# Performance work log

Hardware: AMD Instinct MI355X
Metric: run time of the kernel (lower is better)

The kernel has to match this reference:

```python
import jax, jax.numpy as jnp
import numpy as np

V, D, L, H, T = 32000, 1024, 4, 16, 1024
DH = D // H
SCALE = DH ** -0.5
FF = 4 * D
R = 2  # n_rounds


def setup_inputs() -> dict:
    key = jax.random.key(0)
    ks = iter(jax.random.split(key, 32))
    s = 0.02
    nrm = lambda shape: jax.random.normal(next(ks), shape, dtype=jnp.float32) * s
    inp = {
        "x": jax.random.randint(next(ks), (2, T), 0, V),
        "embed": nrm((V, D)),
        "pos_embed": nrm((T, D)),
        "Wqkv": nrm((L, R, 3 * D, D)),
        "bqkv": jnp.zeros((L, R, 3 * D), jnp.float32),
        "Wo": nrm((L, D, D)),
        "bo": jnp.zeros((L, D), jnp.float32),
        "Wg": nrm((L, D, 2 * D)),
        "bg": jnp.zeros((L, D), jnp.float32),
        "ln1_g": jnp.ones((L, D), jnp.float32),
        "ln1_b": jnp.zeros((L, D), jnp.float32),
        "W1": nrm((L, FF, D)),
        "b1": jnp.zeros((L, FF), jnp.float32),
        "W2": nrm((L, D, FF)),
        "b2": jnp.zeros((L, D), jnp.float32),
        "ln2_g": jnp.ones((L, D), jnp.float32),
        "ln2_b": jnp.zeros((L, D), jnp.float32),
        "lnf_g": jnp.ones((D,), jnp.float32),
        "lnf_b": jnp.zeros((D,), jnp.float32),
    }
    return inp


def _ln(h, g, b, eps=1e-5):
    m = jnp.mean(h, axis=-1, keepdims=True)
    v = jnp.mean((h - m) ** 2, axis=-1, keepdims=True)
    return (h - m) * jax.lax.rsqrt(v + eps) * g + b


def _attend(h, W, b, mask):
    B, Tq, _ = h.shape
    qkv = (h @ W.T + b).reshape(B, Tq, 3, H, DH)
    q, k, v = qkv[:, :, 0], qkv[:, :, 1], qkv[:, :, 2]  # [B,T,H,DH]
    scores = jnp.einsum("bqhd,bkhd->bhqk", q, k) * SCALE
    scores = jnp.where(mask, scores, -jnp.inf)
    a = jax.nn.softmax(scores, axis=-1)
    return jnp.einsum("bhqk,bkhd->bqhd", a, v).reshape(B, Tq, D)


def reference(x, embed, pos_embed, Wqkv, bqkv, Wo, bo, Wg, bg,
              ln1_g, ln1_b, W1, b1, W2, b2, ln2_g, ln2_b, lnf_g, lnf_b):
    B, Tq = x.shape
    mask = jnp.tril(jnp.ones((Tq, Tq), dtype=bool))
    h = embed[x] + pos_embed[jnp.arange(Tq)]
    for l in range(L):
        n1 = _ln(h, ln1_g[l], ln1_b[l])
        pred = _attend(n1, Wqkv[l, 0], bqkv[l, 0], mask)
        cum = pred
        out = pred
        # boosted round 2: attend on residual, gate the correction
        corr = _attend(n1 - cum, Wqkv[l, 1], bqkv[l, 1], mask)
        gate = jax.nn.sigmoid(jnp.concatenate([cum, corr], axis=-1) @ Wg[l].T + bg[l])
        gated = gate * corr
        out = out + gated
        h = h + (out @ Wo[l].T + bo[l])
        n2 = _ln(h, ln2_g[l], ln2_b[l])
        ff = jax.nn.gelu(n2 @ W1[l].T + b1[l], approximate=False) @ W2[l].T + b2[l]
        h = h + ff
    return _ln(h, lnf_g, lnf_b) @ embed.T  # tied head, no bias
```

## Files before the change

kernel.cpp:

```cpp
#include <hip/hip_runtime.h>
#include <math.h>

#define D_  1024
#define T_  1024
#define B_  2
#define H_  16
#define DH_ 64
#define L_  4
#define FF_ 4096
#define V_  32000
#define M_  2048

typedef _Float16 f16;
typedef _Float16 f16x8 __attribute__((ext_vector_type(8)));
typedef _Float16 f16x4 __attribute__((ext_vector_type(4)));
typedef _Float16 f16x2 __attribute__((ext_vector_type(2)));
typedef float    fx4  __attribute__((ext_vector_type(4)));

__global__ __launch_bounds__(256) void f2h_k(const float* __restrict__ in, f16* __restrict__ out) {
    const long i = ((long)blockIdx.x * 256 + threadIdx.x) * 4;
    const float4 v = *(const float4*)(in + i);
    f16x4 o = { (f16)v.x, (f16)v.y, (f16)v.z, (f16)v.w };
    *(f16x4*)(out + i) = o;
}

__global__ __launch_bounds__(256) void embed_k(const int* __restrict__ x, const float* __restrict__ emb,
                                               const float* __restrict__ pos, float* __restrict__ h) {
    const long m = blockIdx.x;
    const int  t = threadIdx.x;
    const long tok = x[m];
    const long pt  = m & (T_ - 1);
    const float4 e = ((const float4*)(emb + tok * D_))[t];
    const float4 p = ((const float4*)(pos + pt * D_))[t];
    ((float4*)(h + m * D_))[t] = make_float4(e.x + p.x, e.y + p.y, e.z + p.z, e.w + p.w);
}

__global__ __launch_bounds__(256) void ln_k(const float* __restrict__ x, const float* __restrict__ g,
                                            const float* __restrict__ b, float* __restrict__ of,
                                            f16* __restrict__ oh) {
    const long m = blockIdx.x;
    const int  t = threadIdx.x;
    const int  wave = t >> 6, lane = t & 63;
    __shared__ float red1[4], red2[4];
    const float4 v = ((const float4*)(x + m * D_))[t];
    float s = v.x + v.y + v.z + v.w;
#pragma unroll
    for (int off = 32; off; off >>= 1) s += __shfl_xor(s, off, 64);
    if (lane == 0) red1[wave] = s;
    __syncthreads();
    const float mean = (red1[0] + red1[1] + red1[2] + red1[3]) * (1.0f / 1024.0f);
    const float d0 = v.x - mean, d1 = v.y - mean, d2 = v.z - mean, d3 = v.w - mean;
    float s2 = d0 * d0 + d1 * d1 + d2 * d2 + d3 * d3;
#pragma unroll
    for (int off = 32; off; off >>= 1) s2 += __shfl_xor(s2, off, 64);
    if (lane == 0) red2[wave] = s2;
    __syncthreads();
    const float var  = (red2[0] + red2[1] + red2[2] + red2[3]) * (1.0f / 1024.0f);
    const float rstd = rsqrtf(var + 1e-5f);
    const float4 gv = ((const float4*)g)[t];
    const float4 bv = ((const float4*)b)[t];
    const float o0 = d0 * rstd * gv.x + bv.x;
    const float o1 = d1 * rstd * gv.y + bv.y;
    const float o2 = d2 * rstd * gv.z + bv.z;
    const float o3 = d3 * rstd * gv.w + bv.w;
    if (of) ((float4*)(of + m * D_))[t] = make_float4(o0, o1, o2, o3);
    if (oh) { f16x4 o = { (f16)o0, (f16)o1, (f16)o2, (f16)o3 }; *(f16x4*)(oh + m * D_ + t * 4) = o; }
}

__global__ __launch_bounds__(256) void sub_k(const float* __restrict__ a, const float* __restrict__ b,
                                             f16* __restrict__ o) {
    const long i = ((long)blockIdx.x * 256 + threadIdx.x) * 4;
    const float4 va = *(const float4*)(a + i);
    const float4 vb = *(const float4*)(b + i);
    f16x4 o4 = { (f16)(va.x - vb.x), (f16)(va.y - vb.y), (f16)(va.z - vb.z), (f16)(va.w - vb.w) };
    *(f16x4*)(o + i) = o4;
}

__global__ __launch_bounds__(256) void cat_k(const float* __restrict__ p, const float* __restrict__ c,
                                             f16* __restrict__ o) {
    const long i = ((long)blockIdx.x * 256 + threadIdx.x) * 4;
    const long m = i >> 11;
    const int  j = (int)(i & 2047);
    const float* src = (j < 1024) ? (p + m * 1024 + j) : (c + m * 1024 + (j - 1024));
    const float4 v = *(const float4*)src;
    f16x4 o4 = { (f16)v.x, (f16)v.y, (f16)v.z, (f16)v.w };
    *(f16x4*)(o + i) = o4;
}

__global__ __launch_bounds__(256) void gate_k(const float* __restrict__ p, const float* __restrict__ c,
                                              const float* __restrict__ gl, f16* __restrict__ o) {
    const long i = ((long)blockIdx.x * 256 + threadIdx.x) * 4;
    const float4 vp = *(const float4*)(p + i);
    const float4 vc = *(const float4*)(c + i);
    const float4 vg = *(const float4*)(gl + i);
    const float s0 = 1.0f / (1.0f + __expf(-vg.x));
    const float s1 = 1.0f / (1.0f + __expf(-vg.y));
    const float s2 = 1.0f / (1.0f + __expf(-vg.z));
    const float s3 = 1.0f / (1.0f + __expf(-vg.w));
    f16x4 o4 = { (f16)(vp.x + s0 * vc.x), (f16)(vp.y + s1 * vc.y),
                 (f16)(vp.z + s2 * vc.z), (f16)(vp.w + s3 * vc.w) };
    *(f16x4*)(o + i) = o4;
}

template<int BN>
__global__ __launch_bounds__(256)
void gemm_bt(const f16* __restrict__ A, const f16* __restrict__ Wt,
             const float* __restrict__ bias, const float* __restrict__ resid,
             float* __restrict__ Cf, f16* __restrict__ Ch,
             int N, int K, int gelu) {
    __shared__ __align__(16) f16 As[3][128 * 32];
    __shared__ __align__(16) f16 Bs[3][BN * 32];
    const int tid  = threadIdx.x;
    const int wave = tid >> 6;
    const int lane = tid & 63;

    const int nbm = gridDim.y;
    const int nbn = gridDim.x;
    int bi = blockIdx.y * nbn + blockIdx.x;
    const int nwg = nbm * nbn;
    if ((nwg & 7) == 0) bi = (bi & 7) * (nwg >> 3) + (bi >> 3);
    const long bm = bi % nbm;
    const long bn = bi / nbm;

    const int wm = (wave >> 1) * 64;
    const int wn = (wave & 1) * (BN / 2);
    constexpr int NJ = BN / 32;

    fx4 acc[4][NJ] = {};

    const int c0 = wave * 2;
    const int r0 = c0 * 16 + (lane >> 2);
    const int cc = ((lane & 3) ^ ((lane >> 3) & 3)) * 8;
    const f16* a0 = A + ((long)bm * 128 + r0) * K + cc;
    const f16* a1 = A + ((long)bm * 128 + r0 + 16) * K + cc;

    const f16* b0;
    const f16* b1 = nullptr;
    if constexpr (BN == 128) {
        b0 = Wt + ((long)bn * 128 + r0) * K + cc;
        b1 = Wt + ((long)bn * 128 + r0 + 16) * K + cc;
    } else {
        b0 = Wt + ((long)bn * 64 + wave * 16 + (lane >> 2)) * K + cc;
    }

    const int NT = K >> 5;

    auto STAGE = [&](int kt) {
        const int k0 = kt * 32;
        const int bf3 = kt % 3;
        __builtin_amdgcn_global_load_lds((const __attribute__((address_space(1))) void*)(a0 + k0),
                                         (__attribute__((address_space(3))) void*)&As[bf3][c0 * 512], 16, 0, 0);
        __builtin_amdgcn_global_load_lds((const __attribute__((address_space(1))) void*)(a1 + k0),
                                         (__attribute__((address_space(3))) void*)&As[bf3][(c0 + 1) * 512], 16, 0, 0);
        if constexpr (BN == 128) {
            __builtin_amdgcn_global_load_lds((const __attribute__((address_space(1))) void*)(b0 + k0),
                                             (__attribute__((address_space(3))) void*)&Bs[bf3][c0 * 512], 16, 0, 0);
            __builtin_amdgcn_global_load_lds((const __attribute__((address_space(1))) void*)(b1 + k0),
                                             (__attribute__((address_space(3))) void*)&Bs[bf3][(c0 + 1) * 512], 16, 0, 0);
        } else {
            __builtin_amdgcn_global_load_lds((const __attribute__((address_space(1))) void*)(b0 + k0),
                                             (__attribute__((address_space(3))) void*)&Bs[bf3][wave * 512], 16, 0, 0);
        }
    };

    STAGE(0);
    if (NT > 1) STAGE(1);

    const int lm = lane & 15;
    const int g  = lane >> 4;
    const int koff = (g ^ ((lm >> 1) & 3)) * 8;
    for (int t = 0; t < NT; ++t) {
        if (t + 2 < NT) STAGE(t + 2);
        const int rem = NT - 1 - t;
        if constexpr (BN == 128) {
            if (rem >= 2)      asm volatile("s_waitcnt vmcnt(8)" ::: "memory");
            else if (rem == 1) asm volatile("s_waitcnt vmcnt(4)" ::: "memory");
            else               asm volatile("s_waitcnt vmcnt(0)" ::: "memory");
        } else {
            if (rem >= 2)      asm volatile("s_waitcnt vmcnt(6)" ::: "memory");
            else if (rem == 1) asm volatile("s_waitcnt vmcnt(3)" ::: "memory");
            else               asm volatile("s_waitcnt vmcnt(0)" ::: "memory");
        }
        __builtin_amdgcn_s_barrier();
        __builtin_amdgcn_sched_barrier(0);

        const f16* as = As[t % 3];
        const f16* bs = Bs[t % 3];
        f16x8 af[4], bf[NJ];
#pragma unroll
        for (int i = 0; i < 4; ++i)
            af[i] = *(const f16x8*)&as[(wm + i * 16 + lm) * 32 + koff];
#pragma unroll
        for (int j = 0; j < NJ; ++j)
            bf[j] = *(const f16x8*)&bs[(wn + j * 16 + lm) * 32 + koff];
#pragma unroll
        for (int i = 0; i < 4; ++i)
#pragma unroll
            for (int j = 0; j < NJ; ++j)
                acc[i][j] = __builtin_amdgcn_mfma_f32_16x16x32_f16(af[i], bf[j], acc[i][j], 0, 0, 0);

        asm volatile("s_waitcnt lgkmcnt(0)" ::: "memory");
        __builtin_amdgcn_sched_barrier(0);
        __builtin_amdgcn_s_barrier();
    }

    const long gr_base = bm * 128 + wm + (lane >> 4) * 4;
    const long gc_base = bn * BN + wn + (lane & 15);
#pragma unroll
    for (int i = 0; i < 4; ++i) {
#pragma unroll
        for (int j = 0; j < NJ; ++j) {
            const long gc = gc_base + j * 16;
            const float bv = bias ? bias[gc] : 0.0f;
#pragma unroll
            for (int r = 0; r < 4; ++r) {
                const long gr = gr_base + i * 16 + r;
                float v = acc[i][j][r] + bv;
                if (gelu) v = 0.5f * v * (1.0f + erff(v * 0.70710678118654752f));
                else if (resid) v += resid[gr * (long)N + gc];
                if (Cf) Cf[gr * (long)N + gc] = v;
                if (Ch) Ch[gr * (long)N + gc] = (f16)v;
            }
        }
    }
}

__global__ __launch_bounds__(256) void fattn_k(const f16* __restrict__ qkv, float* __restrict__ out) {
    __shared__ __align__(16) f16 Ks[64 * 72];
    __shared__ __align__(16) f16 Vt[64 * 72];
    __shared__ __align__(16) f16 Pw[4][16 * 72];
    const int tid  = threadIdx.x;
    const int w    = tid >> 6;
    const int lane = tid & 63;
    const int b  = blockIdx.z, h = blockIdx.y;
    const int qt = (gridDim.x - 1) - blockIdx.x;
    const int q0w = qt * 64 + w * 16;
    const int g  = lane >> 4;
    const int lm = lane & 15;

    const long qrow = ((long)(b * T_ + q0w + lm)) * (3 * D_) + h * DH_;
    f16x8 af_q[2];
    af_q[0] = *(const f16x8*)(qkv + qrow + g * 8);
    af_q[1] = *(const f16x8*)(qkv + qrow + 32 + g * 8);

    float m_r[4], l_r[4];
    fx4 acc_o[4] = {};
#pragma unroll
    for (int r = 0; r < 4; ++r) { m_r[r] = -INFINITY; l_r[r] = 0.0f; }

    const int srow = tid >> 2;
    const int scol = (tid & 3) * 16;
    const long kbase = ((long)(b * T_)) * (3 * D_) + D_ + h * DH_ + scol;
    const int vm  = tid >> 3;
    const int vd0 = (tid & 7) * 8;
    const long vbase = ((long)(b * T_)) * (3 * D_) + 2 * D_ + h * DH_ + vd0;

    f16x8 kr0, kr1, vr0, vr1;
    {
        const f16* ks = qkv + kbase + (long)srow * (3 * D_);
        kr0 = *(const f16x8*)(ks);
        kr1 = *(const f16x8*)(ks + 8);
        const f16* va = qkv + vbase + (long)(2 * vm) * (3 * D_);
        vr0 = *(const f16x8*)(va);
        vr1 = *(const f16x8*)(va + 3 * D_);
    }

    const int nkb = qt + 1;
    for (int it = 0; it < nkb; ++it) {
        const int kb = it * 64;
        __syncthreads();
        *(f16x8*)&Ks[srow * 72 + scol]     = kr0;
        *(f16x8*)&Ks[srow * 72 + scol + 8] = kr1;
#pragma unroll
        for (int j = 0; j < 8; ++j) {
            const int d = vd0 + j;
            const int col = (2 * vm) ^ (((d >> 2) & 7) << 3);
            f16x2 pr = { vr0[j], vr1[j] };
            *(f16x2*)&Vt[d * 72 + col] = pr;
        }
        __syncthreads();

        if (it + 1 < nkb) {
            const int kb2 = kb + 64;
            const f16* ks = qkv + kbase + (long)(kb2 + srow) * (3 * D_);
            kr0 = *(const f16x8*)(ks);
            kr1 = *(const f16x8*)(ks + 8);
            const f16* va = qkv + vbase + (long)(kb2 + 2 * vm) * (3 * D_);
            vr0 = *(const f16x8*)(va);
            vr1 = *(const f16x8*)(va + 3 * D_);
        }

        fx4 sc[4];
#pragma unroll
        for (int kt = 0; kt < 4; ++kt) {
            fx4 c = {};
#pragma unroll
            for (int kk = 0; kk < 2; ++kk) {
                f16x8 bf = *(const f16x8*)&Ks[(kt * 16 + lm) * 72 + kk * 32 + g * 8];
                c = __builtin_amdgcn_mfma_f32_16x16x32_f16(af_q[kk], bf, c, 0, 0, 0);
            }
            sc[kt] = c * 0.125f;
        }
        if (kb == qt * 64) {
#pragma unroll
            for (int kt = 0; kt < 4; ++kt) {
                const int key_g = kb + kt * 16 + lm;
#pragma unroll
                for (int r = 0; r < 4; ++r)
                    if (key_g > q0w + g * 4 + r) sc[kt][r] = -INFINITY;
            }
        }

        float mnew[4], pscale[4];
#pragma unroll
        for (int r = 0; r < 4; ++r) {
            float tm = fmaxf(fmaxf(sc[0][r], sc[1][r]), fmaxf(sc[2][r], sc[3][r]));
#pragma unroll
            for (int off = 8; off; off >>= 1) tm = fmaxf(tm, __shfl_xor(tm, off, 64));
            mnew[r]   = fmaxf(m_r[r], tm);
            pscale[r] = __expf(m_r[r] - mnew[r]);
        }
        float psum[4] = {};
#pragma unroll
        for (int kt = 0; kt < 4; ++kt) {
#pragma unroll
            for (int r = 0; r < 4; ++r) {
                const float p = __expf(sc[kt][r] - mnew[r]);
                sc[kt][r] = p;
                psum[r] += p;
            }
        }
#pragma unroll
        for (int r = 0; r < 4; ++r) {
#pragma unroll
            for (int off = 8; off; off >>= 1) psum[r] += __shfl_xor(psum[r], off, 64);
            l_r[r] = l_r[r] * pscale[r] + psum[r];
            m_r[r] = mnew[r];
        }
#pragma unroll
        for (int nt = 0; nt < 4; ++nt)
#pragma unroll
            for (int r = 0; r < 4; ++r) acc_o[nt][r] *= pscale[r];

        f16* P = Pw[w];
#pragma unroll
        for (int kt = 0; kt < 4; ++kt)
#pragma unroll
            for (int r = 0; r < 4; ++r)
                P[(g * 4 + r) * 72 + kt * 16 + lm] = (f16)sc[kt][r];

#pragma unroll
        for (int kc = 0; kc < 2; ++kc) {
            f16x8 ap = *(const f16x8*)&P[lm * 72 + kc * 32 + g * 8];
#pragma unroll
            for (int nt = 0; nt < 4; ++nt) {
                const int d = nt * 16 + lm;
                const int col = (kc * 32 + g * 8) ^ (((d >> 2) & 7) << 3);
                f16x8 bv = *(const f16x8*)&Vt[d * 72 + col];
                acc_o[nt] = __builtin_amdgcn_mfma_f32_16x16x32_f16(ap, bv, acc_o[nt], 0, 0, 0);
            }
        }
    }

    const long obase = ((long)(b * T_ + q0w + g * 4)) * D_ + h * DH_ + lm;
#pragma unroll
    for (int r = 0; r < 4; ++r) {
        const float inv = 1.0f / l_r[r];
#pragma unroll
        for (int nt = 0; nt < 4; ++nt)
            out[obase + (long)r * D_ + nt * 16] = acc_o[nt][r] * inv;
    }
}

extern "C" void kernel_launch(void* const* d_in, const int* in_sizes, int n_in,
                              void* d_out, int out_size, void* d_ws, size_t ws_size,
                              hipStream_t stream) {
    const int*   x    = (const int*)d_in[0];
    const float* emb  = (const float*)d_in[1];
    const float* pos  = (const float*)d_in[2];
    const float* Wqkv = (const float*)d_in[3];
    const float* bqkv = (const float*)d_in[4];
    const float* Wo   = (const float*)d_in[5];
    const float* bo   = (const float*)d_in[6];
    const float* Wg   = (const float*)d_in[7];
    const float* bg   = (const float*)d_in[8];
    const float* ln1g = (const float*)d_in[9];
    const float* ln1b = (const float*)d_in[10];
    const float* W1   = (const float*)d_in[11];
    const float* b1   = (const float*)d_in[12];
    const float* W2   = (const float*)d_in[13];
    const float* b2   = (const float*)d_in[14];
    const float* ln2g = (const float*)d_in[15];
    const float* ln2b = (const float*)d_in[16];
    const float* lnfg = (const float*)d_in[17];
    const float* lnfb = (const float*)d_in[18];
    float* out = (float*)d_out;

    char* ws = (char*)d_ws;
    size_t off = 0;
    auto alloc = [&](size_t bytes) -> void* {
        off = (off + 255) & ~(size_t)255;
        void* p = ws + off;
        off += bytes;
        return p;
    };
    float* h    = (float*)alloc((size_t)M_ * D_ * 4);
    float* n1f  = (float*)alloc((size_t)M_ * D_ * 4);
    float* pred = (float*)alloc((size_t)M_ * D_ * 4);
    float* corr = (float*)alloc((size_t)M_ * D_ * 4);
    float* glin = (float*)alloc((size_t)M_ * D_ * 4);
    f16* qkvh  = (f16*)alloc((size_t)M_ * 3 * D_ * 2);
    f16* ab    = (f16*)alloc((size_t)M_ * D_ * 2);
    f16* catb  = (f16*)alloc((size_t)M_ * 2 * D_ * 2);
    f16* ffh   = (f16*)alloc((size_t)M_ * FF_ * 2);
    f16* embh  = (f16*)alloc((size_t)V_ * D_ * 2);
    f16* wqkvh = (f16*)alloc((size_t)L_ * 2 * 3 * D_ * D_ * 2);
    f16* woh   = (f16*)alloc((size_t)L_ * D_ * D_ * 2);
    f16* wgh   = (f16*)alloc((size_t)L_ * D_ * 2 * D_ * 2);
    f16* w1h   = (f16*)alloc((size_t)L_ * FF_ * D_ * 2);
    f16* w2h   = (f16*)alloc((size_t)L_ * D_ * FF_ * 2);

    auto cvt = [&](const float* src, f16* dst, long n) {
        f2h_k<<<dim3((unsigned)(n / 1024)), dim3(256), 0, stream>>>(src, dst);
    };
    cvt(emb,  embh,  (long)V_ * D_);
    cvt(Wqkv, wqkvh, (long)L_ * 2 * 3 * D_ * D_);
    cvt(Wo,   woh,   (long)L_ * D_ * D_);
    cvt(Wg,   wgh,   (long)L_ * D_ * 2 * D_);
    cvt(W1,   w1h,   (long)L_ * FF_ * D_);
    cvt(W2,   w2h,   (long)L_ * D_ * FF_);

    embed_k<<<dim3(M_), dim3(256), 0, stream>>>(x, emb, pos, h);

    auto gemm = [&](const f16* A, const f16* Wt, const float* bias, const float* resid,
                    float* Cf, f16* Ch, int N, int K, int gelu) {
        if (N <= 1024)
            gemm_bt<64><<<dim3(N / 64, M_ / 128), dim3(256), 0, stream>>>(A, Wt, bias, resid, Cf, Ch, N, K, gelu);
        else
            gemm_bt<128><<<dim3(N / 128, M_ / 128), dim3(256), 0, stream>>>(A, Wt, bias, resid, Cf, Ch, N, K, gelu);
    };

    for (int l = 0; l < L_; ++l) {
        ln_k<<<dim3(M_), 256, 0, stream>>>(h, ln1g + l * D_, ln1b + l * D_, n1f, ab);
        gemm(ab, wqkvh + (size_t)(l * 2 + 0) * 3 * D_ * D_, bqkv + (l * 2 + 0) * 3 * D_,
             nullptr, nullptr, qkvh, 3 * D_, D_, 0);
        fattn_k<<<dim3(T_ / 64, H_, B_), 256, 0, stream>>>(qkvh, pred);
        sub_k<<<dim3(M_ * D_ / 1024), 256, 0, stream>>>(n1f, pred, ab);
        gemm(ab, wqkvh + (size_t)(l * 2 + 1) * 3 * D_ * D_, bqkv + (l * 2 + 1) * 3 * D_,
             nullptr, nullptr, qkvh, 3 * D_, D_, 0);
        fattn_k<<<dim3(T_ / 64, H_, B_), 256, 0, stream>>>(qkvh, corr);
        cat_k<<<dim3(M_ * 2 * D_ / 1024), 256, 0, stream>>>(pred, corr, catb);
        gemm(catb, wgh + (size_t)l * D_ * 2 * D_, bg + l * D_, nullptr, glin, nullptr, D_, 2 * D_, 0);
        gate_k<<<dim3(M_ * D_ / 1024), 256, 0, stream>>>(pred, corr, glin, ab);
        gemm(ab, woh + (size_t)l * D_ * D_, bo + l * D_, h, h, nullptr, D_, D_, 0);
        ln_k<<<dim3(M_), 256, 0, stream>>>(h, ln2g + l * D_, ln2b + l * D_, nullptr, ab);
        gemm(ab, w1h + (size_t)l * FF_ * D_, b1 + l * FF_, nullptr, nullptr, ffh, FF_, D_, 1);
        gemm(ffh, w2h + (size_t)l * D_ * FF_, b2 + l * D_, h, h, nullptr, D_, FF_, 0);
    }
    ln_k<<<dim3(M_), 256, 0, stream>>>(h, lnfg, lnfb, nullptr, ab);
    gemm(ab, embh, nullptr, nullptr, out, nullptr, V_, D_, 0);
}
```

Baseline: 2.200 ms.

## Vectorize GEMM epilogue via LDS transpose; use 128-key attention tiles with causal skip

The GEMM epilogue now stages each 16x16 accumulator tile through per-wave LDS scratch. Each lane then writes 4 contiguous outputs with vector loads and stores for bias, residual, fp32 and fp16 outputs, replacing scattered scalar stores. The flash attention kernel processes 128 keys per iteration instead of 64, halving barrier and loop overhead. It also skips MFMA and softmax work for fully masked 16-key subtiles on the diagonal block. This costs more LDS and registers per block and extra waitcnt syncs in the epilogue, and could reduce occupancy.

```diff
diff --git a/kernel.cpp b/kernel.cpp
--- a/kernel.cpp
+++ b/kernel.cpp
@@ -204,31 +204,51 @@
         __builtin_amdgcn_s_barrier();
     }
 
-    const long gr_base = bm * 128 + wm + (lane >> 4) * 4;
-    const long gc_base = bn * BN + wn + (lane & 15);
+    float* esc = (float*)&As[0][0] + (size_t)wave * 320;
+    const int erow = lane >> 2;
+    const int ecg  = (lane & 3) * 4;
+    const long gr0 = bm * 128 + wm;
+    const long gc0 = bn * BN + wn;
 #pragma unroll
     for (int i = 0; i < 4; ++i) {
 #pragma unroll
         for (int j = 0; j < NJ; ++j) {
-            const long gc = gc_base + j * 16;
-            const float bv = bias ? bias[gc] : 0.0f;
-#pragma unroll
-            for (int r = 0; r < 4; ++r) {
-                const long gr = gr_base + i * 16 + r;
-                float v = acc[i][j][r] + bv;
-                if (gelu) v = 0.5f * v * (1.0f + erff(v * 0.70710678118654752f));
-                else if (resid) v += resid[gr * (long)N + gc];
-                if (Cf) Cf[gr * (long)N + gc] = v;
-                if (Ch) Ch[gr * (long)N + gc] = (f16)v;
+#pragma unroll
+            for (int r = 0; r < 4; ++r)
+                esc[(g * 4 + r) * 20 + lm] = acc[i][j][r];
+            asm volatile("s_waitcnt lgkmcnt(0)" ::: "memory");
+            __builtin_amdgcn_sched_barrier(0);
+            const fx4 q = *(const fx4*)&esc[erow * 20 + ecg];
+            asm volatile("s_waitcnt lgkmcnt(0)" ::: "memory");
+            __builtin_amdgcn_sched_barrier(0);
+            const long row = gr0 + i * 16 + erow;
+            const long col = gc0 + j * 16 + ecg;
+            fx4 v = q;
+            if (bias) {
+                const fx4 b4 = *(const fx4*)&bias[col];
+                v[0] += b4[0]; v[1] += b4[1]; v[2] += b4[2]; v[3] += b4[3];
+            }
+            if (gelu) {
+#pragma unroll
+                for (int e = 0; e < 4; ++e)
+                    v[e] = 0.5f * v[e] * (1.0f + erff(v[e] * 0.70710678118654752f));
+            } else if (resid) {
+                const fx4 rz = *(const fx4*)&resid[row * (long)N + col];
+                v[0] += rz[0]; v[1] += rz[1]; v[2] += rz[2]; v[3] += rz[3];
+            }
+            if (Cf) *(fx4*)&Cf[row * (long)N + col] = v;
+            if (Ch) {
+                f16x4 hq = { (f16)v[0], (f16)v[1], (f16)v[2], (f16)v[3] };
+                *(f16x4*)&Ch[row * (long)N + col] = hq;
             }
         }
     }
 }
 
 __global__ __launch_bounds__(256) void fattn_k(const f16* __restrict__ qkv, float* __restrict__ out) {
-    __shared__ __align__(16) f16 Ks[64 * 72];
-    __shared__ __align__(16) f16 Vt[64 * 72];
-    __shared__ __align__(16) f16 Pw[4][16 * 72];
+    __shared__ __align__(16) f16 Ks[128 * 72];
+    __shared__ __align__(16) f16 Vt[64 * 136];
+    __shared__ __align__(16) f16 Pw[4][16 * 136];
     const int tid  = threadIdx.x;
     const int w    = tid >> 6;
     const int lane = tid & 63;
@@ -248,73 +268,95 @@
 #pragma unroll
     for (int r = 0; r < 4; ++r) { m_r[r] = -INFINITY; l_r[r] = 0.0f; }
 
-    const int srow = tid >> 2;
-    const int scol = (tid & 3) * 16;
-    const long kbase = ((long)(b * T_)) * (3 * D_) + D_ + h * DH_ + scol;
-    const int vm  = tid >> 3;
-    const int vd0 = (tid & 7) * 8;
+    const int krow = tid >> 1;
+    const int kdh  = (tid & 1) * 32;
+    const long kbase = ((long)(b * T_)) * (3 * D_) + D_ + h * DH_ + kdh;
+    const int vm  = tid >> 2;
+    const int vd0 = (tid & 3) * 16;
     const long vbase = ((long)(b * T_)) * (3 * D_) + 2 * D_ + h * DH_ + vd0;
 
-    f16x8 kr0, kr1, vr0, vr1;
+    const int nit = (qt >> 1) + 1;
+
+    f16x8 kr0, kr1, kr2, kr3, vr0, vr1, vr2, vr3;
     {
-        const f16* ks = qkv + kbase + (long)srow * (3 * D_);
+        const f16* ks = qkv + kbase + (long)krow * (3 * D_);
         kr0 = *(const f16x8*)(ks);
         kr1 = *(const f16x8*)(ks + 8);
+        kr2 = *(const f16x8*)(ks + 16);
+        kr3 = *(const f16x8*)(ks + 24);
         const f16* va = qkv + vbase + (long)(2 * vm) * (3 * D_);
         vr0 = *(const f16x8*)(va);
-        vr1 = *(const f16x8*)(va + 3 * D_);
-    }
-
-    const int nkb = qt + 1;
-    for (int it = 0; it < nkb; ++it) {
-        const int kb = it * 64;
+        vr1 = *(const f16x8*)(va + 8);
+        vr2 = *(const f16x8*)(va + 3 * D_);
+        vr3 = *(const f16x8*)(va + 3 * D_ + 8);
+    }
+
+    for (int it = 0; it < nit; ++it) {
+        const int kb = it * 128;
         __syncthreads();
-        *(f16x8*)&Ks[srow * 72 + scol]     = kr0;
-        *(f16x8*)&Ks[srow * 72 + scol + 8] = kr1;
-#pragma unroll
-        for (int j = 0; j < 8; ++j) {
-            const int d = vd0 + j;
+        *(f16x8*)&Ks[krow * 72 + kdh]      = kr0;
+        *(f16x8*)&Ks[krow * 72 + kdh + 8]  = kr1;
+        *(f16x8*)&Ks[krow * 72 + kdh + 16] = kr2;
+        *(f16x8*)&Ks[krow * 72 + kdh + 24] = kr3;
+#pragma unroll
+        for (int jj = 0; jj < 16; ++jj) {
+            const int d = vd0 + jj;
+            const f16 va_ = (jj < 8) ? vr0[jj] : vr1[jj - 8];
+            const f16 vb_ = (jj < 8) ? vr2[jj] : vr3[jj - 8];
             const int col = (2 * vm) ^ (((d >> 2) & 7) << 3);
-            f16x2 pr = { vr0[j], vr1[j] };
-            *(f16x2*)&Vt[d * 72 + col] = pr;
+            f16x2 pr = { va_, vb_ };
+            *(f16x2*)&Vt[d * 136 + col] = pr;
         }
         __syncthreads();
 
-        if (it + 1 < nkb) {
-            const int kb2 = kb + 64;
-            const f16* ks = qkv + kbase + (long)(kb2 + srow) * (3 * D_);
+        if (it + 1 < nit) {
+            const int kb2 = kb + 128;
+            const f16* ks = qkv + kbase + (long)(kb2 + krow) * (3 * D_);
             kr0 = *(const f16x8*)(ks);
             kr1 = *(const f16x8*)(ks + 8);
+            kr2 = *(const f16x8*)(ks + 16);
+            kr3 = *(const f16x8*)(ks + 24);
             const f16* va = qkv + vbase + (long)(kb2 + 2 * vm) * (3 * D_);
             vr0 = *(const f16x8*)(va);
-            vr1 = *(const f16x8*)(va + 3 * D_);
-        }
-
-        fx4 sc[4];
-#pragma unroll
-        for (int kt = 0; kt < 4; ++kt) {
-            fx4 c = {};
-#pragma unroll
-            for (int kk = 0; kk < 2; ++kk) {
-                f16x8 bf = *(const f16x8*)&Ks[(kt * 16 + lm) * 72 + kk * 32 + g * 8];
-                c = __builtin_amdgcn_mfma_f32_16x16x32_f16(af_q[kk], bf, c, 0, 0, 0);
-            }
-            sc[kt] = c * 0.125f;
-        }
-        if (kb == qt * 64) {
-#pragma unroll
-            for (int kt = 0; kt < 4; ++kt) {
-                const int key_g = kb + kt * 16 + lm;
-#pragma unroll
-                for (int r = 0; r < 4; ++r)
-                    if (key_g > q0w + g * 4 + r) sc[kt][r] = -INFINITY;
+            vr1 = *(const f16x8*)(va + 8);
+            vr2 = *(const f16x8*)(va + 3 * D_);
+            vr3 = *(const f16x8*)(va + 3 * D_ + 8);
+        }
+
+        const int qmax = q0w + 15;
+        int nact = qmax - kb + 1; if (nact > 128) nact = 128;
+        const int nkt = (nact + 15) >> 4;
+        const int nkc = (nact + 31) >> 5;
+        const bool diag = (kb + 127 > q0w);
+
+        fx4 sc[8];
+#pragma unroll
+        for (int kt = 0; kt < 8; ++kt) {
+            if (kt < nkt) {
+                fx4 c = {};
+#pragma unroll
+                for (int kk = 0; kk < 2; ++kk) {
+                    f16x8 bf = *(const f16x8*)&Ks[(kt * 16 + lm) * 72 + kk * 32 + g * 8];
+                    c = __builtin_amdgcn_mfma_f32_16x16x32_f16(af_q[kk], bf, c, 0, 0, 0);
+                }
+                c *= 0.125f;
+                if (diag) {
+                    const int key_g = kb + kt * 16 + lm;
+#pragma unroll
+                    for (int r = 0; r < 4; ++r)
+                        if (key_g > q0w + g * 4 + r) c[r] = -INFINITY;
+                }
+                sc[kt] = c;
             }
         }
 
         float mnew[4], pscale[4];
 #pragma unroll
         for (int r = 0; r < 4; ++r) {
-            float tm = fmaxf(fmaxf(sc[0][r], sc[1][r]), fmaxf(sc[2][r], sc[3][r]));
+            float tm = -INFINITY;
+#pragma unroll
+            for (int kt = 0; kt < 8; ++kt)
+                if (kt < nkt) tm = fmaxf(tm, sc[kt][r]);
 #pragma unroll
             for (int off = 8; off; off >>= 1) tm = fmaxf(tm, __shfl_xor(tm, off, 64));
             mnew[r]   = fmaxf(m_r[r], tm);
@@ -322,12 +364,14 @@
         }
         float psum[4] = {};
 #pragma unroll
-        for (int kt = 0; kt < 4; ++kt) {
-#pragma unroll
-            for (int r = 0; r < 4; ++r) {
-                const float p = __expf(sc[kt][r] - mnew[r]);
-                sc[kt][r] = p;
-                psum[r] += p;
+        for (int kt = 0; kt < 8; ++kt) {
+            if (kt < nkt) {
+#pragma unroll
+                for (int r = 0; r < 4; ++r) {
+                    const float p = __expf(sc[kt][r] - mnew[r]);
+                    sc[kt][r] = p;
+                    psum[r] += p;
+                }
             }
         }
 #pragma unroll
@@ -344,20 +388,29 @@
 
         f16* P = Pw[w];
 #pragma unroll
-        for (int kt = 0; kt < 4; ++kt)
-#pragma unroll
-            for (int r = 0; r < 4; ++r)
-                P[(g * 4 + r) * 72 + kt * 16 + lm] = (f16)sc[kt][r];
-
-#pragma unroll
-        for (int kc = 0; kc < 2; ++kc) {
-            f16x8 ap = *(const f16x8*)&P[lm * 72 + kc * 32 + g * 8];
-#pragma unroll
-            for (int nt = 0; nt < 4; ++nt) {
-                const int d = nt * 16 + lm;
-                const int col = (kc * 32 + g * 8) ^ (((d >> 2) & 7) << 3);
-                f16x8 bv = *(const f16x8*)&Vt[d * 72 + col];
-                acc_o[nt] = __builtin_amdgcn_mfma_f32_16x16x32_f16(ap, bv, acc_o[nt], 0, 0, 0);
+        for (int kt = 0; kt < 8; ++kt) {
+            if (kt < nkt) {
+#pragma unroll
+                for (int r = 0; r < 4; ++r)
+                    P[(g * 4 + r) * 136 + kt * 16 + lm] = (f16)sc[kt][r];
+            } else if (kt == nkt) {
+#pragma unroll
+                for (int r = 0; r < 4; ++r)
+                    P[(g * 4 + r) * 136 + kt * 16 + lm] = (f16)0.0f;
+            }
+        }
+
+#pragma unroll
+        for (int kc = 0; kc < 4; ++kc) {
+            if (kc < nkc) {
+                f16x8 ap = *(const f16x8*)&P[lm * 136 + kc * 32 + g * 8];
+#pragma unroll
+                for (int nt = 0; nt < 4; ++nt) {
+                    const int d = nt * 16 + lm;
+                    const int col = (kc * 32 + g * 8) ^ (((d >> 2) & 7) << 3);
+                    f16x8 bv = *(const f16x8*)&Vt[d * 136 + col];
+                    acc_o[nt] = __builtin_amdgcn_mfma_f32_16x16x32_f16(ap, bv, acc_o[nt], 0, 0, 0);
+                }
             }
         }
     }
```

New measurement: 2.149 ms. 1.02x faster.
